# Kernel tuning notes

Measured on AMD Instinct MI355X. Metric: run time of the kernel, lower is better.

Reference implementation:

```python
import jax, jax.numpy as jnp
import numpy as np

B, L, D, H = 2, 2048, 2048, 16
DH = D // H
SCALE = 1.0 / float(np.sqrt(DH))


def setup_inputs() -> dict:
    key = jax.random.key(0)
    ks = jax.random.split(key, 5)
    std = 1.0 / float(np.sqrt(D))
    return {
        "x": jax.random.normal(ks[0], (B, L, D), dtype=jnp.float32),
        "W_q": jax.random.normal(ks[1], (D, D), dtype=jnp.float32) * std,
        "W_k": jax.random.normal(ks[2], (D, D), dtype=jnp.float32) * std,
        "W_v": jax.random.normal(ks[3], (D, D), dtype=jnp.float32) * std,
        "W_o": jax.random.normal(ks[4], (D, D), dtype=jnp.float32) * std,
    }


def _split_heads(t):
    # (B, L, D) -> (B, H, L, DH)
    b, l, _ = t.shape
    return t.reshape(b, l, H, DH).transpose(0, 2, 1, 3)


def reference(x, W_q, W_k, W_v, W_o):
    # nn.Linear(bias=False): y = x @ W.T
    q = _split_heads(x @ W_q.T)  # (B,H,L,DH)
    k = _split_heads(x @ W_k.T)
    v = _split_heads(x @ W_v.T)
    scores = jnp.einsum("bhqd,bhkd->bhqk", q, k) * SCALE  # (B,H,L,L)
    causal = jnp.arange(L)[:, None] >= jnp.arange(L)[None, :]  # True = keep
    scores = jnp.where(causal[None, None], scores, -jnp.inf)
    attn = jax.nn.softmax(scores, axis=-1)
    y = jnp.einsum("bhqk,bhkd->bhqd", attn, v)  # (B,H,L,DH)
    y = y.transpose(0, 2, 1, 3).reshape(B, L, D)  # merge heads
    return y @ W_o.T
```

## Files before the change

### kernel.cpp

```cpp
#include <hip/hip_runtime.h>
#include <hip/hip_bf16.h>
#include <stdint.h>

typedef unsigned short u16;
typedef __bf16 bf16x8 __attribute__((ext_vector_type(8)));
typedef float f32x4 __attribute__((ext_vector_type(4)));

#define SEQ    2048
#define DMODEL 2048
#define NHEAD  16
#define DHEAD  128
#define QSCALE (0.088388347648318447f * 1.4426950408889634f)

__device__ __forceinline__ u16 f2bf(float f){
  uint32_t u = __float_as_uint(f);
  u += 0x7FFFu + ((u >> 16) & 1u);
  return (u16)(u >> 16);
}

__device__ __forceinline__ void gload_lds16(const u16* g, u16* l){
  __builtin_amdgcn_global_load_lds((const __attribute__((address_space(1))) void*)g,
                                   (__attribute__((address_space(3))) void*)l,
                                   16, 0, 0);
}

__global__ __launch_bounds__(256) void cvt_all(const float* __restrict__ x,
    const float* __restrict__ Wq, const float* __restrict__ Wk,
    const float* __restrict__ Wv, const float* __restrict__ Wo,
    u16* __restrict__ dst){
  int gid = blockIdx.x * 256 + threadIdx.x;
  const float* s; int idx;
  if (gid < 2097152){ s = x; idx = gid; }
  else {
    int j = gid - 2097152;
    int z = j >> 20; idx = j & 0xFFFFF;
    s = (z==0) ? Wq : (z==1) ? Wk : (z==2) ? Wv : Wo;
  }
  float4 v = reinterpret_cast<const float4*>(s)[idx];
  ushort4 o;
  o.x = f2bf(v.x); o.y = f2bf(v.y); o.z = f2bf(v.z); o.w = f2bf(v.w);
  reinterpret_cast<ushort4*>(dst)[gid] = o;
}

__device__ __forceinline__ void stageA(const u16* __restrict__ G, int grow0, int kt,
                                       int half, u16* lds, int w, int lane){
  #pragma unroll
  for (int j = 0; j < 2; ++j){
    int q   = w*2 + j;
    int r0  = ((q & 8) << 4) + half*64 + (q & 7)*8;
    int row = r0 + (lane >> 3);
    int sc  = (lane & 7) ^ (row & 7);
    gload_lds16(G + (size_t)(grow0 + row)*DMODEL + kt*64 + sc*8, lds + r0*64);
  }
}

__device__ __forceinline__ bf16x8 ldsf(const u16* lds, int row, int c){
  return *reinterpret_cast<const bf16x8*>(lds + row*64 + (((c ^ (row & 7)) & 7) << 3));
}

template<int MH>
__device__ __forceinline__ void load_a(bf16x8 (&a)[4][2], const u16* LA,
                                       int wr, int ln, int g){
  #pragma unroll
  for (int m = 0; m < 4; ++m){
    int row = wr*128 + MH*64 + m*16 + ln;
    a[m][0] = ldsf(LA, row, g);
    a[m][1] = ldsf(LA, row, 4 + g);
  }
}

__device__ __forceinline__ void phase_pre(){
  __builtin_amdgcn_s_barrier();
  __builtin_amdgcn_sched_barrier(0);
}

__device__ __forceinline__ void stageB192(const u16* __restrict__ G, int grow0,
    int kt, u16* lds, int w, int lane){
  #pragma unroll
  for (int j = 0; j < 3; ++j){
    int q   = w*3 + j;
    int r0  = q*8;
    int row = r0 + (lane >> 3);
    int sc  = (lane & 7) ^ (row & 7);
    gload_lds16(G + (size_t)(grow0 + row)*DMODEL + kt*64 + sc*8, lds + r0*64);
  }
}

__device__ __forceinline__ void load_b192(bf16x8 (&b)[3][2], const u16* LB,
                                          int wc, int ln, int g){
  #pragma unroll
  for (int n = 0; n < 3; ++n){
    int row = wc*48 + n*16 + ln;
    b[n][0] = ldsf(LB, row, g);
    b[n][1] = ldsf(LB, row, 4 + g);
  }
}

template<int MH>
__device__ __forceinline__ void mfma8x3(f32x4 (&acc)[8][3], bf16x8 (&a)[4][2],
                                        bf16x8 (&b)[3][2]){
  __builtin_amdgcn_s_setprio(1);
  #pragma unroll
  for (int m = 0; m < 4; ++m)
    #pragma unroll
    for (int n = 0; n < 3; ++n){
      acc[MH*4+m][n] = __builtin_amdgcn_mfma_f32_16x16x32_bf16(
          a[m][0], b[n][0], acc[MH*4+m][n], 0, 0, 0);
      acc[MH*4+m][n] = __builtin_amdgcn_mfma_f32_16x16x32_bf16(
          a[m][1], b[n][1], acc[MH*4+m][n], 0, 0, 0);
    }
  __builtin_amdgcn_s_setprio(0);
}

__global__ __launch_bounds__(512, 1) void gemm_qkv192(const u16* __restrict__ A,
    const u16* __restrict__ Wall, u16* __restrict__ Q, u16* __restrict__ Kb,
    u16* __restrict__ Vt){
  __shared__ __align__(16) u16 ldsA[2][256*64];
  __shared__ __align__(16) u16 ldsB[2][192*64];
  const int tid = threadIdx.x, w = tid >> 6, lane = tid & 63;
  const int g = lane >> 4, ln = lane & 15;
  const int wr = w >> 2, wc = w & 3;
  const int bid = blockIdx.x;
  const int swz = (bid & 7)*64 + (bid >> 3);
  const int nt = swz >> 4, mt = swz & 15;
  const int bm = mt*256, bnl = nt*192;
  f32x4 acc[8][3];
  {
    const f32x4 z4 = {0.f,0.f,0.f,0.f};
    #pragma unroll
    for (int i = 0; i < 8; ++i)
      #pragma unroll
      for (int j = 0; j < 3; ++j) acc[i][j] = z4;
  }
  stageA  (A,    bm,  0, 0, ldsA[0], w, lane);
  stageA  (A,    bm,  0, 1, ldsA[0], w, lane);
  stageB192(Wall, bnl, 0,    ldsB[0], w, lane);
  stageA  (A,    bm,  1, 0, ldsA[1], w, lane);
  asm volatile("s_waitcnt vmcnt(2)" ::: "memory");
  __builtin_amdgcn_s_barrier();

  bf16x8 a[4][2], b[3][2];
  const int NT = DMODEL/64;
  for (int t = 0; t < NT; ++t){
    const int cur = t & 1;
    const u16* LA = ldsA[cur];
    const u16* LB = ldsB[cur];
    load_a<0>(a, LA, wr, ln, g);
    load_b192(b, LB, wc, ln, g);
    if (t+1 < NT){
      stageA  (A,    bm,  t+1, 1, ldsA[cur^1], w, lane);
      stageB192(Wall, bnl, t+1,    ldsB[cur^1], w, lane);
    }
    phase_pre();
    mfma8x3<0>(acc, a, b);
    __builtin_amdgcn_s_barrier();
    load_a<1>(a, LA, wr, ln, g);
    if (t+2 < NT) stageA(A, bm, t+2, 0, ldsA[cur], w, lane);
    if (t < NT-2) { asm volatile("s_waitcnt vmcnt(2)" ::: "memory"); }
    else          { asm volatile("s_waitcnt vmcnt(0)" ::: "memory"); }
    phase_pre();
    mfma8x3<1>(acc, a, b);
    __builtin_amdgcn_s_barrier();
  }

  #pragma unroll
  for (int mf = 0; mf < 8; ++mf)
    #pragma unroll
    for (int nf = 0; nf < 3; ++nf){
      int col = bnl + wc*48 + nf*16 + ln;
      int z   = col >> 11;
      int c2  = col & 2047;
      if (z < 2){
        u16* C = (z == 0) ? Q : Kb;
        const float sc = (z == 0) ? QSCALE : 1.0f;
        #pragma unroll
        for (int i = 0; i < 4; ++i){
          int row = bm + wr*128 + mf*16 + g*4 + i;
          C[(size_t)row*DMODEL + c2] = f2bf(acc[mf][nf][i] * sc);
        }
      } else {
        int row0 = bm + wr*128 + mf*16 + g*4;
        int bb   = row0 >> 11, lt = row0 & (SEQ-1);
        ushort4 pk;
        pk.x = f2bf(acc[mf][nf][0]); pk.y = f2bf(acc[mf][nf][1]);
        pk.z = f2bf(acc[mf][nf][2]); pk.w = f2bf(acc[mf][nf][3]);
        *reinterpret_cast<ushort4*>(Vt + (size_t)(bb*DMODEL + c2)*SEQ + lt) = pk;
      }
    }
}

__device__ __forceinline__ void stageB3(const u16* __restrict__ G, int grow0,
    int kt, u16* lds, int w, int lane){
  #pragma unroll
  for (int j = 0; j < 2; ++j){
    int q   = w*2 + j;
    int r0  = q*8;
    int row = r0 + (lane >> 3);
    int sc  = (lane & 7) ^ (row & 7);
    gload_lds16(G + (size_t)(grow0 + row)*DMODEL + kt*64 + sc*8, lds + r0*64);
  }
}

__device__ __forceinline__ void load_b3(bf16x8 (&b)[2][2], const u16* LB,
                                        int wc, int ln, int g){
  #pragma unroll
  for (int n = 0; n < 2; ++n){
    int row = wc*32 + n*16 + ln;
    b[n][0] = ldsf(LB, row, g);
    b[n][1] = ldsf(LB, row, 4 + g);
  }
}

template<int MH>
__device__ __forceinline__ void mfma8x2(f32x4 (&acc)[8][2], bf16x8 (&a)[4][2],
                                        bf16x8 (&b)[2][2]){
  __builtin_amdgcn_s_setprio(1);
  #pragma unroll
  for (int m = 0; m < 4; ++m)
    #pragma unroll
    for (int n = 0; n < 2; ++n){
      acc[MH*4+m][n] = __builtin_amdgcn_mfma_f32_16x16x32_bf16(
          a[m][0], b[n][0], acc[MH*4+m][n], 0, 0, 0);
      acc[MH*4+m][n] = __builtin_amdgcn_mfma_f32_16x16x32_bf16(
          a[m][1], b[n][1], acc[MH*4+m][n], 0, 0, 0);
    }
  __builtin_amdgcn_s_setprio(0);
}

__global__ __launch_bounds__(512, 2) void gemm_out3(const u16* __restrict__ A,
    const u16* __restrict__ Wo, float* __restrict__ C){
  __shared__ __align__(16) u16 ldsA[2][256*64];
  __shared__ __align__(16) u16 ldsB[2][128*64];
  const int tid = threadIdx.x, w = tid >> 6, lane = tid & 63;
  const int g = lane >> 4, ln = lane & 15;
  const int wr = w >> 2, wc = w & 3;
  const int bid = blockIdx.x;
  const int x = bid & 7, s = bid >> 3;
  const int mt = s >> 1, nt = 2*x + (s & 1);
  const int bm = mt*256, bnl = nt << 7;
  f32x4 acc[8][2];
  {
    const f32x4 z4 = {0.f,0.f,0.f,0.f};
    #pragma unroll
    for (int i = 0; i < 8; ++i){ acc[i][0] = z4; acc[i][1] = z4; }
  }
  stageA (A,  bm,  0, 0, ldsA[0], w, lane);
  stageA (A,  bm,  0, 1, ldsA[0], w, lane);
  stageB3(Wo, bnl, 0,    ldsB[0], w, lane);
  stageA (A,  bm,  1, 0, ldsA[1], w, lane);
  asm volatile("s_waitcnt vmcnt(2)" ::: "memory");
  __builtin_amdgcn_s_barrier();

  bf16x8 a[4][2], b[2][2];
  const int NT = DMODEL/64;
  for (int t = 0; t < NT; ++t){
    const int cur = t & 1;
    const u16* LA = ldsA[cur];
    const u16* LB = ldsB[cur];
    load_a<0>(a, LA, wr, ln, g);
    load_b3(b, LB, wc, ln, g);
    if (t+1 < NT){
      stageA (A,  bm,  t+1, 1, ldsA[cur^1], w, lane);
      stageB3(Wo, bnl, t+1,    ldsB[cur^1], w, lane);
    }
    phase_pre();
    mfma8x2<0>(acc, a, b);
    __builtin_amdgcn_s_barrier();
    load_a<1>(a, LA, wr, ln, g);
    if (t+2 < NT) stageA(A, bm, t+2, 0, ldsA[cur], w, lane);
    if (t < NT-2) { asm volatile("s_waitcnt vmcnt(2)" ::: "memory"); }
    else          { asm volatile("s_waitcnt vmcnt(0)" ::: "memory"); }
    phase_pre();
    mfma8x2<1>(acc, a, b);
    __builtin_amdgcn_s_barrier();
  }

  #pragma unroll
  for (int mf = 0; mf < 8; ++mf)
    #pragma unroll
    for (int nf = 0; nf < 2; ++nf){
      int col = bnl + wc*32 + nf*16 + ln;
      #pragma unroll
      for (int i = 0; i < 4; ++i){
        int row = bm + wr*128 + mf*16 + g*4 + i;
        C[(size_t)row*DMODEL + col] = acc[mf][nf][i];
      }
    }
}

__device__ __forceinline__ void attn_stageK(const u16* __restrict__ Kb,
    u16* Kt, int b, int h, int kb, int w, int lane){
  #pragma unroll
  for (int is = 0; is < 4; ++is){
    int o = w*4096 + is*1024 + lane*16;
    int row = o >> 8;
    int sc  = ((o >> 4) & 15) ^ (row & 7);
    gload_lds16(Kb + (size_t)(b*SEQ + kb + row)*DMODEL + h*DHEAD + sc*8,
                Kt + w*2048 + is*512);
  }
}
__device__ __forceinline__ void attn_stageV(const u16* __restrict__ Vtb,
    u16* Vt, int bh, int kb, int w, int lane){
  #pragma unroll
  for (int is = 0; is < 4; ++is){
    int o = w*4096 + is*1024 + lane*16;
    int row = o >> 7;
    int sc  = ((o >> 4) & 7) ^ (row & 7);
    gload_lds16(Vtb + (size_t)(bh*DHEAD + row)*SEQ + kb + sc*8,
                Vt + w*2048 + is*512);
  }
}

template<bool MASKED>
__device__ __forceinline__ void attn_qkt_sm(const u16* Kt, u16* Pw,
    const bf16x8 (&qf)[2][4], f32x4 (&yacc)[2][8],
    float (&mrun)[2], float (&lrun)[2],
    int kb, int qg0, int g, int ln){
  #pragma unroll
  for (int qc = 0; qc < 2; ++qc){
    f32x4 st[4];
    __builtin_amdgcn_s_setprio(1);
    #pragma unroll
    for (int kt = 0; kt < 4; ++kt){
      f32x4 accs = {0.f,0.f,0.f,0.f};
      #pragma unroll
      for (int c = 0; c < 4; ++c){
        int row = kt*16 + ln;
        int ch  = (c*4 + g) ^ (row & 7);
        bf16x8 kf = *reinterpret_cast<const bf16x8*>(Kt + row*128 + ch*8);
        accs = __builtin_amdgcn_mfma_f32_16x16x32_bf16(kf, qf[qc][c], accs, 0, 0, 0);
      }
      st[kt] = accs;
    }
    __builtin_amdgcn_s_setprio(0);

    const int qg = qg0 + qc*16;
    float p[16];
    float tmax = -1e30f;
    #pragma unroll
    for (int kt = 0; kt < 4; ++kt)
      #pragma unroll
      for (int i = 0; i < 4; ++i){
        float s = st[kt][i];
        if (MASKED && (kb + kt*16 + g*4 + i) > qg) s = -1e30f;
        p[kt*4+i] = s;
        tmax = fmaxf(tmax, s);
      }
    tmax = fmaxf(tmax, __shfl_xor(tmax, 16));
    tmax = fmaxf(tmax, __shfl_xor(tmax, 32));

    if (!__all(tmax - mrun[qc] <= 11.5f)){
      float mn = fmaxf(mrun[qc], tmax);
      float fr = __builtin_amdgcn_exp2f(mrun[qc] - mn);
      lrun[qc] *= fr;
      float fi[4];
      #pragma unroll
      for (int i = 0; i < 4; ++i) fi[i] = __shfl(fr, g*4 + i);
      #pragma unroll
      for (int dt = 0; dt < 8; ++dt)
        #pragma unroll
        for (int i = 0; i < 4; ++i) yacc[qc][dt][i] *= fi[i];
      mrun[qc] = mn;
    }
    float psum = 0.f;
    #pragma unroll
    for (int j = 0; j < 16; ++j){
      p[j] = __builtin_amdgcn_exp2f(p[j] - mrun[qc]);
      psum += p[j];
    }
    psum += __shfl_xor(psum, 16);
    psum += __shfl_xor(psum, 32);
    lrun[qc] += psum;

    char* pb = reinterpret_cast<char*>(Pw + qc*1024);
    #pragma unroll
    for (int kt = 0; kt < 4; ++kt)
      #pragma unroll
      for (int pr = 0; pr < 2; ++pr){
        uint32_t pk = (uint32_t)f2bf(p[kt*4 + 2*pr]) |
                      ((uint32_t)f2bf(p[kt*4 + 2*pr + 1]) << 16);
        int byte = (kt*16 + g*4 + 2*pr)*2;
        int ch   = (byte >> 4) ^ (ln & 7);
        int addr = ln*128 + (ch << 4) + (byte & 15);
        *reinterpret_cast<uint32_t*>(pb + addr) = pk;
      }
  }
}

__device__ __forceinline__ void attn_pv(const u16* Vt, const u16* Pw,
                                        f32x4 (&yacc)[2][8], int g, int ln){
  __builtin_amdgcn_s_setprio(1);
  #pragma unroll
  for (int kc = 0; kc < 2; ++kc){
    int chp = (kc*4 + g) ^ (ln & 7);
    bf16x8 pf0 = *reinterpret_cast<const bf16x8*>(Pw +        ln*64 + chp*8);
    bf16x8 pf1 = *reinterpret_cast<const bf16x8*>(Pw + 1024 + ln*64 + chp*8);
    #pragma unroll
    for (int dt = 0; dt < 8; ++dt){
      int row = dt*16 + ln;
      int chv = (kc*4 + g) ^ (row & 7);
      bf16x8 vf = *reinterpret_cast<const bf16x8*>(Vt + row*64 + chv*8);
      yacc[0][dt] = __builtin_amdgcn_mfma_f32_16x16x32_bf16(pf0, vf, yacc[0][dt], 0, 0, 0);
      yacc[1][dt] = __builtin_amdgcn_mfma_f32_16x16x32_bf16(pf1, vf, yacc[1][dt], 0, 0, 0);
    }
  }
  __builtin_amdgcn_s_setprio(0);
}

__global__ __launch_bounds__(256, 2) void attn_fwd(const u16* __restrict__ Qb,
    const u16* __restrict__ Kb, const u16* __restrict__ Vtb, u16* __restrict__ Yb){
  __shared__ __align__(16) u16 Kt[2][64*128];
  __shared__ __align__(16) u16 Vt[2][128*64];
  __shared__ __align__(16) u16 Pl[4][2048];
  const int tid = threadIdx.x, w = tid >> 6, lane = tid & 63;
  const int g = lane >> 4, ln = lane & 15;
  const int bid = blockIdx.x;
  const int xcd = bid & 7, idx = bid >> 3;
  const int slot = idx >> 4, j = idx & 15;
  const int x = (j & 1) ? (15 - (j >> 1)) : (j >> 1);
  const int bh = (slot < 2) ? (xcd*2 + slot) : (xcd*2 + 14 + slot);
  const int b = bh >> 4, h = bh & 15;
  const int qb = (bh < 16) ? x : (15 - x);
  const int qw = qb*128 + w*32;
  const int qg0 = qw + ln;
  const int NT = 2*qb + 2;

  bf16x8 qf[2][4];
  #pragma unroll
  for (int qc = 0; qc < 2; ++qc){
    const u16* qp = Qb + (size_t)(b*SEQ + qw + qc*16 + ln)*DMODEL + h*DHEAD + g*8;
    #pragma unroll
    for (int c = 0; c < 4; ++c) qf[qc][c] = *reinterpret_cast<const bf16x8*>(qp + c*32);
  }
  float mrun[2] = {-1e30f, -1e30f}, lrun[2] = {0.f, 0.f};
  f32x4 yacc[2][8];
  {
    const f32x4 z4 = {0.f,0.f,0.f,0.f};
    #pragma unroll
    for (int qc = 0; qc < 2; ++qc)
      #pragma unroll
      for (int dt = 0; dt < 8; ++dt) yacc[qc][dt] = z4;
  }
  u16* Pw = &Pl[w][0];

  attn_stageK(Kb, &Kt[0][0], b, h, 0, w, lane);
  attn_stageV(Vtb, &Vt[0][0], bh, 0, w, lane);
  asm volatile("s_waitcnt vmcnt(0)" ::: "memory");
  __builtin_amdgcn_s_barrier();

  int cur = 0;
  for (int t = 0; t < NT; ++t){
    const int kb = t*64;
    if (t+1 < NT){
      attn_stageK(Kb, &Kt[cur^1][0], b, h, kb + 64, w, lane);
      attn_stageV(Vtb, &Vt[cur^1][0], bh, kb + 64, w, lane);
    }
    bool active = true;
    if (t < NT-2){
      attn_qkt_sm<false>(&Kt[cur][0], Pw, qf, yacc, mrun, lrun, kb, qg0, g, ln);
    } else if (t == NT-2){
      if (w >= 2) attn_qkt_sm<false>(&Kt[cur][0], Pw, qf, yacc, mrun, lrun, kb, qg0, g, ln);
      else        attn_qkt_sm<true >(&Kt[cur][0], Pw, qf, yacc, mrun, lrun, kb, qg0, g, ln);
    } else {
      if (w >= 2) attn_qkt_sm<true >(&Kt[cur][0], Pw, qf, yacc, mrun, lrun, kb, qg0, g, ln);
      else        active = false;
    }
    if (active) attn_pv(&Vt[cur][0], Pw, yacc, g, ln);
    asm volatile("s_waitcnt vmcnt(0) lgkmcnt(0)" ::: "memory");
    __builtin_amdgcn_s_barrier();
    cur ^= 1;
  }

  #pragma unroll
  for (int qc = 0; qc < 2; ++qc){
    float inv[4];
    #pragma unroll
    for (int i = 0; i < 4; ++i){
      float li = __shfl(lrun[qc], g*4 + i);
      inv[i] = __builtin_amdgcn_rcpf(li);
    }
    #pragma unroll
    for (int dt = 0; dt < 8; ++dt)
      #pragma unroll
      for (int i = 0; i < 4; ++i){
        Yb[(size_t)(b*SEQ + qw + qc*16 + g*4 + i)*DMODEL + h*DHEAD + dt*16 + ln] =
            f2bf(yacc[qc][dt][i] * inv[i]);
      }
  }
}

extern "C" void kernel_launch(void* const* d_in, const int* in_sizes, int n_in,
                              void* d_out, int out_size, void* d_ws, size_t ws_size,
                              hipStream_t stream) {
  const float* x  = (const float*)d_in[0];
  const float* Wq = (const float*)d_in[1];
  const float* Wk = (const float*)d_in[2];
  const float* Wv = (const float*)d_in[3];
  const float* Wo = (const float*)d_in[4];
  float* out = (float*)d_out;

  char* ws = (char*)d_ws;
  u16* xb  = (u16*)(ws +          0);
  u16* Wqb = (u16*)(ws + 16777216);
  u16* Wob = (u16*)(ws + 41943040);
  u16* Qb  = (u16*)(ws + 50331648);
  u16* Kb  = (u16*)(ws + 67108864);
  u16* Vtb = (u16*)(ws + 83886080);
  u16* Yb  = (u16*)(ws + 100663296);

  cvt_all<<<dim3(24576), 256, 0, stream>>>(x, Wq, Wk, Wv, Wo, xb);

  gemm_qkv192<<<dim3(512), 512, 0, stream>>>(xb, Wqb, Qb, Kb, Vtb);

  attn_fwd<<<dim3(512), 256, 0, stream>>>(Qb, Kb, Vtb, Yb);

  gemm_out3<<<dim3(256), 512, 0, stream>>>(Yb, Wob, out);
}
```

Baseline: 250.6 us.

## Use 32x32x16 MFMA for QK^T with per-lane row softmax state

The QK^T step now uses 32x32x16 bf16 MFMA over the whole 32-query by 64-key tile, instead of sixteen 16x16x32 tiles split into two query chunks. Each lane owns one query row, so the running max and sum become scalars. The cross-lane reductions drop from two shuffles to one, and each K fragment load feeds a larger instruction. The cost is a remapping of the P writes to LDS and of the rescale factors into the 16x16 PV accumulator layout. That remapping raises register pressure from two 16-wide accumulators plus 32 probabilities per lane.

```diff
diff --git a/kernel.cpp b/kernel.cpp
--- a/kernel.cpp
+++ b/kernel.cpp
@@ -5,6 +5,7 @@
 typedef unsigned short u16;
 typedef __bf16 bf16x8 __attribute__((ext_vector_type(8)));
 typedef float f32x4 __attribute__((ext_vector_type(4)));
+typedef float f32x16 __attribute__((ext_vector_type(16)));
 
 #define SEQ    2048
 #define DMODEL 2048
@@ -313,77 +314,82 @@
 
 template<bool MASKED>
 __device__ __forceinline__ void attn_qkt_sm(const u16* Kt, u16* Pw,
-    const bf16x8 (&qf)[2][4], f32x4 (&yacc)[2][8],
-    float (&mrun)[2], float (&lrun)[2],
-    int kb, int qg0, int g, int ln){
-  #pragma unroll
-  for (int qc = 0; qc < 2; ++qc){
-    f32x4 st[4];
-    __builtin_amdgcn_s_setprio(1);
-    #pragma unroll
-    for (int kt = 0; kt < 4; ++kt){
-      f32x4 accs = {0.f,0.f,0.f,0.f};
-      #pragma unroll
-      for (int c = 0; c < 4; ++c){
-        int row = kt*16 + ln;
-        int ch  = (c*4 + g) ^ (row & 7);
-        bf16x8 kf = *reinterpret_cast<const bf16x8*>(Kt + row*128 + ch*8);
-        accs = __builtin_amdgcn_mfma_f32_16x16x32_bf16(kf, qf[qc][c], accs, 0, 0, 0);
-      }
-      st[kt] = accs;
-    }
-    __builtin_amdgcn_s_setprio(0);
-
-    const int qg = qg0 + qc*16;
-    float p[16];
-    float tmax = -1e30f;
-    #pragma unroll
-    for (int kt = 0; kt < 4; ++kt)
-      #pragma unroll
-      for (int i = 0; i < 4; ++i){
-        float s = st[kt][i];
-        if (MASKED && (kb + kt*16 + g*4 + i) > qg) s = -1e30f;
-        p[kt*4+i] = s;
-        tmax = fmaxf(tmax, s);
-      }
-    tmax = fmaxf(tmax, __shfl_xor(tmax, 16));
-    tmax = fmaxf(tmax, __shfl_xor(tmax, 32));
-
-    if (!__all(tmax - mrun[qc] <= 11.5f)){
-      float mn = fmaxf(mrun[qc], tmax);
-      float fr = __builtin_amdgcn_exp2f(mrun[qc] - mn);
-      lrun[qc] *= fr;
+    const bf16x8 (&qf2)[8], f32x4 (&yacc)[2][8],
+    float& mrun, float& lrun,
+    int kb, int qgl, int g, int lane){
+  const int krow = lane & 31, khi = lane >> 5;
+  f32x16 accA = {0.f,0.f,0.f,0.f,0.f,0.f,0.f,0.f,0.f,0.f,0.f,0.f,0.f,0.f,0.f,0.f};
+  f32x16 accB = accA;
+  __builtin_amdgcn_s_setprio(1);
+  #pragma unroll
+  for (int c2 = 0; c2 < 8; ++c2){
+    int rowA = krow;
+    int rowB = 32 + krow;
+    int pre  = c2*2 + khi;
+    bf16x8 kfA = *reinterpret_cast<const bf16x8*>(Kt + rowA*128 + ((pre ^ (rowA & 7)) << 3));
+    bf16x8 kfB = *reinterpret_cast<const bf16x8*>(Kt + rowB*128 + ((pre ^ (rowB & 7)) << 3));
+    accA = __builtin_amdgcn_mfma_f32_32x32x16_bf16(kfA, qf2[c2], accA, 0, 0, 0);
+    accB = __builtin_amdgcn_mfma_f32_32x32x16_bf16(kfB, qf2[c2], accB, 0, 0, 0);
+  }
+  __builtin_amdgcn_s_setprio(0);
+
+  float pA[16], pB[16];
+  float tmax = -1e30f;
+  #pragma unroll
+  for (int r = 0; r < 16; ++r){
+    int kl = (r & 3) + 8*(r >> 2) + 4*khi;
+    float sA = accA[r], sB = accB[r];
+    if (MASKED && (kb + kl)      > qgl) sA = -1e30f;
+    if (MASKED && (kb + 32 + kl) > qgl) sB = -1e30f;
+    pA[r] = sA; pB[r] = sB;
+    tmax = fmaxf(tmax, fmaxf(sA, sB));
+  }
+  tmax = fmaxf(tmax, __shfl_xor(tmax, 32));
+
+  if (!__all(tmax - mrun <= 11.5f)){
+    float mn = fmaxf(mrun, tmax);
+    float fr = __builtin_amdgcn_exp2f(mrun - mn);
+    lrun *= fr;
+    #pragma unroll
+    for (int qc = 0; qc < 2; ++qc){
       float fi[4];
       #pragma unroll
-      for (int i = 0; i < 4; ++i) fi[i] = __shfl(fr, g*4 + i);
+      for (int i = 0; i < 4; ++i) fi[i] = __shfl(fr, qc*16 + g*4 + i);
       #pragma unroll
       for (int dt = 0; dt < 8; ++dt)
         #pragma unroll
         for (int i = 0; i < 4; ++i) yacc[qc][dt][i] *= fi[i];
-      mrun[qc] = mn;
-    }
-    float psum = 0.f;
-    #pragma unroll
-    for (int j = 0; j < 16; ++j){
-      p[j] = __builtin_amdgcn_exp2f(p[j] - mrun[qc]);
-      psum += p[j];
-    }
-    psum += __shfl_xor(psum, 16);
-    psum += __shfl_xor(psum, 32);
-    lrun[qc] += psum;
-
-    char* pb = reinterpret_cast<char*>(Pw + qc*1024);
-    #pragma unroll
-    for (int kt = 0; kt < 4; ++kt)
-      #pragma unroll
-      for (int pr = 0; pr < 2; ++pr){
-        uint32_t pk = (uint32_t)f2bf(p[kt*4 + 2*pr]) |
-                      ((uint32_t)f2bf(p[kt*4 + 2*pr + 1]) << 16);
-        int byte = (kt*16 + g*4 + 2*pr)*2;
-        int ch   = (byte >> 4) ^ (ln & 7);
-        int addr = ln*128 + (ch << 4) + (byte & 15);
-        *reinterpret_cast<uint32_t*>(pb + addr) = pk;
-      }
+    }
+    mrun = mn;
+  }
+  float psum = 0.f;
+  #pragma unroll
+  for (int r = 0; r < 16; ++r){
+    pA[r] = __builtin_amdgcn_exp2f(pA[r] - mrun);
+    pB[r] = __builtin_amdgcn_exp2f(pB[r] - mrun);
+    psum += pA[r] + pB[r];
+  }
+  psum += __shfl_xor(psum, 32);
+  lrun += psum;
+
+  const int qloc = krow;
+  char* pb = reinterpret_cast<char*>(Pw + (qloc >> 4)*1024);
+  const int lnp = qloc & 15;
+  #pragma unroll
+  for (int r = 0; r < 16; r += 2){
+    int kl = (r & 3) + 8*(r >> 2) + 4*khi;
+    {
+      uint32_t pk = (uint32_t)f2bf(pA[r]) | ((uint32_t)f2bf(pA[r+1]) << 16);
+      int byte = 2*kl;
+      int ch   = (byte >> 4) ^ (lnp & 7);
+      *reinterpret_cast<uint32_t*>(pb + lnp*128 + (ch << 4) + (byte & 15)) = pk;
+    }
+    {
+      uint32_t pk = (uint32_t)f2bf(pB[r]) | ((uint32_t)f2bf(pB[r+1]) << 16);
+      int byte = 2*(32 + kl);
+      int ch   = (byte >> 4) ^ (lnp & 7);
+      *reinterpret_cast<uint32_t*>(pb + lnp*128 + (ch << 4) + (byte & 15)) = pk;
+    }
   }
 }
 
@@ -422,17 +428,18 @@
   const int b = bh >> 4, h = bh & 15;
   const int qb = (bh < 16) ? x : (15 - x);
   const int qw = qb*128 + w*32;
-  const int qg0 = qw + ln;
+  const int krow = lane & 31, khi = lane >> 5;
+  const int qgl = qw + krow;
   const int NT = 2*qb + 2;
 
-  bf16x8 qf[2][4];
-  #pragma unroll
-  for (int qc = 0; qc < 2; ++qc){
-    const u16* qp = Qb + (size_t)(b*SEQ + qw + qc*16 + ln)*DMODEL + h*DHEAD + g*8;
-    #pragma unroll
-    for (int c = 0; c < 4; ++c) qf[qc][c] = *reinterpret_cast<const bf16x8*>(qp + c*32);
-  }
-  float mrun[2] = {-1e30f, -1e30f}, lrun[2] = {0.f, 0.f};
+  bf16x8 qf2[8];
+  {
+    const u16* qp = Qb + (size_t)(b*SEQ + qw + krow)*DMODEL + h*DHEAD + khi*8;
+    #pragma unroll
+    for (int c2 = 0; c2 < 8; ++c2)
+      qf2[c2] = *reinterpret_cast<const bf16x8*>(qp + c2*16);
+  }
+  float mrun = -1e30f, lrun = 0.f;
   f32x4 yacc[2][8];
   {
     const f32x4 z4 = {0.f,0.f,0.f,0.f};
@@ -457,12 +464,12 @@
     }
     bool active = true;
     if (t < NT-2){
-      attn_qkt_sm<false>(&Kt[cur][0], Pw, qf, yacc, mrun, lrun, kb, qg0, g, ln);
+      attn_qkt_sm<false>(&Kt[cur][0], Pw, qf2, yacc, mrun, lrun, kb, qgl, g, lane);
     } else if (t == NT-2){
-      if (w >= 2) attn_qkt_sm<false>(&Kt[cur][0], Pw, qf, yacc, mrun, lrun, kb, qg0, g, ln);
-      else        attn_qkt_sm<true >(&Kt[cur][0], Pw, qf, yacc, mrun, lrun, kb, qg0, g, ln);
+      if (w >= 2) attn_qkt_sm<false>(&Kt[cur][0], Pw, qf2, yacc, mrun, lrun, kb, qgl, g, lane);
+      else        attn_qkt_sm<true >(&Kt[cur][0], Pw, qf2, yacc, mrun, lrun, kb, qgl, g, lane);
     } else {
-      if (w >= 2) attn_qkt_sm<true >(&Kt[cur][0], Pw, qf, yacc, mrun, lrun, kb, qg0, g, ln);
+      if (w >= 2) attn_qkt_sm<true >(&Kt[cur][0], Pw, qf2, yacc, mrun, lrun, kb, qgl, g, lane);
       else        active = false;
     }
     if (active) attn_pv(&Vt[cur][0], Pw, yacc, g, ln);
@@ -476,7 +483,7 @@
     float inv[4];
     #pragma unroll
     for (int i = 0; i < 4; ++i){
-      float li = __shfl(lrun[qc], g*4 + i);
+      float li = __shfl(lrun, qc*16 + g*4 + i);
       inv[i] = __builtin_amdgcn_rcpf(li);
     }
     #pragma unroll
```

Measured after the change: 323.3 us. 29.0% more time.
